# Kernel optimization log

Measured on AMD Instinct MI355X. Metric: run time of the kernel, lower is better.

The kernel has to match this reference:

```python
import jax, jax.numpy as jnp
import numpy as np

N, E = 100000, 600000
IN, H = 164, 128
NH = 4  # attention heads over embed_dim H//4 = 32


def layer_norm(x, g, b, eps=1e-5):
    m = x.mean(-1, keepdims=True)
    v = x.var(-1, keepdims=True)
    return (x - m) * jax.lax.rsqrt(v + eps) * g + b


def gcn_conv(x, W, b, src, dst, n):
    # PyG GCNConv: add self-loops, symmetric D^{-1/2}(A+I)D^{-1/2} normalization.
    deg = jnp.ones((n,), x.dtype).at[dst].add(1.0)  # degree of A+I on target nodes
    dinv = jax.lax.rsqrt(deg)
    xw = x @ W  # [n, out]
    msg = xw[src] * (dinv[src] * dinv[dst])[:, None]  # gather + edge-norm
    agg = jax.ops.segment_sum(msg, dst, num_segments=n)  # scatter-add
    agg = agg + xw * (dinv * dinv)[:, None]  # self-loop term
    return agg + b


def mha_seq1(x, Wq, bq, Wk, bk, Wv, bv, Wo, bo):
    # nn.MultiheadAttention with seq_len==1: softmax over a single key -> weights==1.
    dh = x.shape[-1] // NH
    q = (x @ Wq + bq).reshape(-1, NH, dh)
    k = (x @ Wk + bk).reshape(-1, NH, dh)
    v = (x @ Wv + bv).reshape(-1, NH, dh)
    scores = jnp.sum(q * k, -1, keepdims=True) / jnp.sqrt(jnp.float32(dh))  # [n,NH,1]
    attn = jax.nn.softmax(scores[..., None], axis=-1)[..., 0]  # all ones, kept for fidelity
    out = (attn * v).reshape(-1, NH * dh)
    return out @ Wo + bo


def setup_inputs() -> dict:
    key = jax.random.key(0)
    ks = jax.random.split(key, 16)

    def kaiming(k, i, o):
        return jax.random.normal(k, (i, o), jnp.float32) * (2.0 / i) ** 0.5

    Ha, Hb, Hc = H, H // 2, H // 4  # 128, 64, 32
    return {
        "x": jax.random.normal(ks[0], (N, IN), jnp.float32),
        "edge_index": jax.random.randint(ks[1], (2, E), 0, N),
        "Wi": kaiming(ks[2], IN, Ha), "bi": jnp.zeros((Ha,), jnp.float32),
        "g1": jnp.ones((Ha,), jnp.float32), "b1": jnp.zeros((Ha,), jnp.float32),
        "Wg1": kaiming(ks[3], Ha, Ha), "bg1": jnp.zeros((Ha,), jnp.float32),
        "Wg2": kaiming(ks[4], Ha, Hb), "bg2": jnp.zeros((Hb,), jnp.float32),
        "g2": jnp.ones((Hb,), jnp.float32), "b2": jnp.zeros((Hb,), jnp.float32),
        "Wg3": kaiming(ks[5], Hb, Hc), "bg3": jnp.zeros((Hc,), jnp.float32),
        "Wq": kaiming(ks[6], Hc, Hc), "bq": jnp.zeros((Hc,), jnp.float32),
        "Wk": kaiming(ks[7], Hc, Hc), "bk": jnp.zeros((Hc,), jnp.float32),
        "Wv": kaiming(ks[8], Hc, Hc), "bv": jnp.zeros((Hc,), jnp.float32),
        "Wo": kaiming(ks[9], Hc, Hc), "bo": jnp.zeros((Hc,), jnp.float32),
        "Wc1": kaiming(ks[10], Hc, H // 8), "bc1": jnp.zeros((H // 8,), jnp.float32),
        "Wc2": kaiming(ks[11], H // 8, 32), "bc2": jnp.zeros((32,), jnp.float32),
        "Wc3": kaiming(ks[12], 32, 1), "bc3": jnp.zeros((1,), jnp.float32),
    }


def reference(x, edge_index, Wi, bi, g1, b1, Wg1, bg1, Wg2, bg2, g2, b2,
              Wg3, bg3, Wq, bq, Wk, bk, Wv, bv, Wo, bo,
              Wc1, bc1, Wc2, bc2, Wc3, bc3):
    src, dst = edge_index[0], edge_index[1]
    n = x.shape[0]
    # dropout layers are identity in eval mode
    h = layer_norm(jax.nn.relu(x @ Wi + bi), g1, b1)
    h1 = jax.nn.relu(gcn_conv(h, Wg1, bg1, src, dst, n)) + h
    h2 = layer_norm(jax.nn.relu(gcn_conv(h1, Wg2, bg2, src, dst, n)), g2, b2)
    h3 = jax.nn.relu(gcn_conv(h2, Wg3, bg3, src, dst, n))
    h3 = mha_seq1(h3, Wq, bq, Wk, bk, Wv, bv, Wo, bo)
    h3 = jax.nn.relu(h3 @ Wc1 + bc1)
    h3 = jax.nn.relu(h3 @ Wc2 + bc2)
    return (h3 @ Wc3 + bc3)[:, 0]
```

## Files before the change

kernel.cpp:

```cpp
#include <hip/hip_runtime.h>


typedef __attribute__((ext_vector_type(8))) _Float16 f16x8;
typedef __attribute__((ext_vector_type(4))) _Float16 f16x4;
typedef __attribute__((ext_vector_type(4))) float f32x4;

#define GLOAD_LDS16(gp, lp)                                        \
  __builtin_amdgcn_global_load_lds(                                \
      (const __attribute__((address_space(1))) void*)(gp),         \
      (__attribute__((address_space(3))) void*)(lp), 16, 0, 0)

static __device__ __forceinline__ void wait_vm0() {
  asm volatile("s_waitcnt vmcnt(0)" ::: "memory");
}
static __device__ __forceinline__ void wait_vm1() {
  asm volatile("s_waitcnt vmcnt(1)" ::: "memory");
}
static __device__ __forceinline__ void wait_vm2() {
  asm volatile("s_waitcnt vmcnt(2)" ::: "memory");
}

__global__ void k_count(const int* __restrict__ dst, int* __restrict__ counts, int e) {
  int i = blockIdx.x * blockDim.x + threadIdx.x;
  if (i < e) atomicAdd(&counts[dst[i]], 1);
}

__global__ __launch_bounds__(256) void k_scan_part(
    const int* __restrict__ counts, int* __restrict__ bsums, int n) {
  int tid = threadIdx.x;
  int i0 = blockIdx.x * 1024 + tid * 4;
  int s = 0;
#pragma unroll
  for (int k = 0; k < 4; k++) { int i = i0 + k; if (i < n) s += counts[i]; }
#pragma unroll
  for (int d = 1; d < 64; d <<= 1) s += __shfl_xor(s, d);
  __shared__ int wsum[4];
  int lane = tid & 63, w = tid >> 6;
  if (lane == 0) wsum[w] = s;
  __syncthreads();
  if (tid == 0) bsums[blockIdx.x] = wsum[0] + wsum[1] + wsum[2] + wsum[3];
}

__global__ __launch_bounds__(128) void k_scan_top(int* __restrict__ bsums, int nb) {
  int tid = threadIdx.x;
  int orig = (tid < nb) ? bsums[tid] : 0;
  int v = orig;
  int lane = tid & 63, w = tid >> 6;
#pragma unroll
  for (int d = 1; d < 64; d <<= 1) { int t = __shfl_up(v, d); if (lane >= d) v += t; }
  __shared__ int ws[2];
  if (lane == 63) ws[w] = v;
  __syncthreads();
  if (w == 1) v += ws[0];
  if (tid < nb) bsums[tid] = v - orig;
}

__global__ __launch_bounds__(256) void k_scan_down(
    int* __restrict__ counts, const int* __restrict__ bsums,
    int* __restrict__ offsets, float* __restrict__ dinv, int n, int e) {
  int tid = threadIdx.x;
  int i0 = blockIdx.x * 1024 + tid * 4;
  int c[4]; int tsum = 0;
#pragma unroll
  for (int k = 0; k < 4; k++) { int i = i0 + k; c[k] = (i < n) ? counts[i] : 0; tsum += c[k]; }
  int v = tsum;
  int lane = tid & 63, w = tid >> 6;
#pragma unroll
  for (int d = 1; d < 64; d <<= 1) { int t = __shfl_up(v, d); if (lane >= d) v += t; }
  __shared__ int wsum[4];
  if (lane == 63) wsum[w] = v;
  __syncthreads();
  int wadd = 0;
#pragma unroll
  for (int q = 0; q < 4; q++) if (q < w) wadd += wsum[q];
  int run = (v - tsum) + wadd + bsums[blockIdx.x];
#pragma unroll
  for (int k = 0; k < 4; k++) {
    int i = i0 + k;
    if (i < n) {
      offsets[i] = run;
      dinv[i] = rsqrtf((float)(c[k] + 1));
      counts[i] = 0;
    }
    run += c[k];
  }
  if (blockIdx.x == 0 && tid == 0) offsets[n] = e;
}

__global__ void k_fill(const int* __restrict__ src, const int* __restrict__ dst,
                       const int* __restrict__ offsets, int* __restrict__ cursor,
                       const float* __restrict__ dinv, int2* __restrict__ csr, int e) {
  int i = blockIdx.x * blockDim.x + threadIdx.x;
  if (i >= e) return;
  int s = src[i], d = dst[i];
  int pos = atomicAdd(&cursor[d], 1);
  csr[offsets[d] + pos] = make_int2(s, __float_as_int(dinv[s] * dinv[d]));
}

__device__ __forceinline__ void pack_hi(const float* __restrict__ W,
                                        _Float16* __restrict__ dst,
                                        int K, int N, int u) {
  int lane = u & 63; int rest = u >> 6; int CT = N >> 4;
  int ct = rest % CT, ks = rest / CT;
  int gcol = ct * 16 + (lane & 15);
  int gk0 = ks * 32 + (lane >> 4) * 8;
  size_t o = (size_t)(ks * CT + ct) * 512 + lane * 8;
#pragma unroll
  for (int i = 0; i < 8; i++) {
    float v = (gk0 + i < K) ? W[(size_t)(gk0 + i) * N + gcol] : 0.0f;
    dst[o + i] = (_Float16)v;
  }
}

__global__ void k_setup(const float* __restrict__ Wi, const float* __restrict__ Wg1,
                        const float* __restrict__ Wg2, const float* __restrict__ Wg3,
                        _Float16* __restrict__ pWi, _Float16* __restrict__ pWg1,
                        _Float16* __restrict__ pWg2, _Float16* __restrict__ pWg3,
                        int* __restrict__ counts, float* __restrict__ zp, int n) {
  int b = blockIdx.x;
  if (b < 25) {
    int t = b * 256 + threadIdx.x;
    if (t < 3072) pack_hi(Wi, pWi, 164, 128, t);
    else if (t < 5120) pack_hi(Wg1, pWg1, 128, 128, t - 3072);
    else if (t < 6144) pack_hi(Wg2, pWg2, 128, 64, t - 5120);
    else if (t < 6400) pack_hi(Wg3, pWg3, 64, 32, t - 6144);
  } else {
    if (b == 25 && threadIdx.x < 64) zp[threadIdx.x] = 0.0f;
    int i = (b - 25) * 256 + threadIdx.x;
    if (i < n) counts[i] = 0;
  }
}

__global__ __launch_bounds__(512, 4) void k_gemm_in(
    const float* __restrict__ x, const _Float16* __restrict__ pB,
    const float* __restrict__ bias, const float* __restrict__ gamma,
    const float* __restrict__ beta, const float* __restrict__ zp,
    _Float16* __restrict__ out, int n) {
  constexpr int N = 128, CT = 8;
  __shared__ __align__(16) float sA[2][128 * 32];
  int tid = threadIdx.x;
  int lane = tid & 63, w = tid >> 6;
  int base = blockIdx.x * 128;
  const f16x8* Bf = (const f16x8*)pB;

  auto stage = [&](int ks, int buf) {
#pragma unroll
    for (int j = 0; j < 2; j++) {
      int q = (j * 8 + w) * 64 + lane;
      int row = q >> 3;
      int c = q & 7;
      int rg = base + row;
      const void* src = (rg < n && (ks < 5 || c == 0))
                            ? (const void*)(x + (size_t)rg * 164 + ks * 32 + c * 4)
                            : (const void*)zp;
      GLOAD_LDS16(src, &sA[buf][(size_t)(j * 8 + w) * 256]);
    }
  };

  f32x4 acc[CT];
#pragma unroll
  for (int c = 0; c < CT; c++) acc[c] = (f32x4)0.0f;

  stage(0, 0);
#pragma unroll
  for (int ks = 0; ks < 6; ks++) {
    if (ks + 1 < 6) { stage(ks + 1, (ks + 1) & 1); wait_vm2(); }
    else wait_vm0();
    __builtin_amdgcn_s_barrier();
    const float4* fr = (const float4*)&sA[ks & 1][((w * 16 + (lane & 15)) * 32) +
                                                 (lane >> 4) * 8];
    float4 u0 = fr[0], u1 = fr[1];
    float v[8] = {u0.x, u0.y, u0.z, u0.w, u1.x, u1.y, u1.z, u1.w};
    f16x8 ah, al;
#pragma unroll
    for (int i = 0; i < 8; i++) {
      ah[i] = (_Float16)v[i];
      al[i] = (_Float16)(v[i] - (float)ah[i]);
    }
#pragma unroll
    for (int c = 0; c < CT; c++) {
      f16x8 b = Bf[(ks * CT + c) * 64 + lane];
      acc[c] = __builtin_amdgcn_mfma_f32_16x16x32_f16(ah, b, acc[c], 0, 0, 0);
      acc[c] = __builtin_amdgcn_mfma_f32_16x16x32_f16(al, b, acc[c], 0, 0, 0);
    }
    __builtin_amdgcn_s_barrier();
  }

  int r0 = (lane >> 4) * 4;
  int li = lane & 15;
  float s1[4] = {0, 0, 0, 0}, s2[4] = {0, 0, 0, 0};
#pragma unroll
  for (int c = 0; c < CT; c++) {
    float bb = bias[c * 16 + li];
#pragma unroll
    for (int r = 0; r < 4; r++) {
      float t = acc[c][r] + bb;
      t = t > 0.0f ? t : 0.0f;
      acc[c][r] = t;
      s1[r] += t;
      s2[r] += t * t;
    }
  }
#pragma unroll
  for (int m = 1; m < 16; m <<= 1) {
#pragma unroll
    for (int r = 0; r < 4; r++) {
      s1[r] += __shfl_xor(s1[r], m);
      s2[r] += __shfl_xor(s2[r], m);
    }
  }
#pragma unroll
  for (int c = 0; c < CT; c++) {
    float gv = gamma[c * 16 + li], bv = beta[c * 16 + li];
#pragma unroll
    for (int r = 0; r < 4; r++) {
      int node = base + w * 16 + r0 + r;
      if (node < n) {
        float mean = s1[r] * (1.0f / N);
        float var = s2[r] * (1.0f / N) - mean * mean;
        float rs = rsqrtf(var + 1e-5f);
        out[(size_t)node * N + c * 16 + li] =
            (_Float16)((acc[c][r] - mean) * rs * gv + bv);
      }
    }
  }
}

template <int K, int N>
__global__ __launch_bounds__(512, 4) void k_gemm_f16(
    const _Float16* __restrict__ A, const _Float16* __restrict__ pB,
    const float* __restrict__ zp, _Float16* __restrict__ out, int n) {
  constexpr int KS = K / 32, CT = N / 16;
  __shared__ __align__(16) _Float16 sA[2][128 * 32];
  int tid = threadIdx.x;
  int lane = tid & 63, w = tid >> 6;
  int base = blockIdx.x * 128;
  const f16x8* Bf = (const f16x8*)pB;

  auto stage = [&](int ks, int buf) {
    int q = w * 64 + lane;
    int row = q >> 2;
    int c = q & 3;
    int rg = base + row;
    const void* src = (rg < n) ? (const void*)(A + (size_t)rg * K + ks * 32 + c * 8)
                               : (const void*)zp;
    GLOAD_LDS16(src, &sA[buf][(size_t)w * 512]);
  };

  f32x4 acc[CT];
#pragma unroll
  for (int c = 0; c < CT; c++) acc[c] = (f32x4)0.0f;

  stage(0, 0);
#pragma unroll
  for (int ks = 0; ks < KS; ks++) {
    if (ks + 1 < KS) { stage(ks + 1, (ks + 1) & 1); wait_vm1(); }
    else wait_vm0();
    __builtin_amdgcn_s_barrier();
    f16x8 av = *(const f16x8*)&sA[ks & 1][((w * 16 + (lane & 15)) * 32) +
                                          (lane >> 4) * 8];
#pragma unroll
    for (int c = 0; c < CT; c++) {
      f16x8 b = Bf[(ks * CT + c) * 64 + lane];
      acc[c] = __builtin_amdgcn_mfma_f32_16x16x32_f16(av, b, acc[c], 0, 0, 0);
    }
    __builtin_amdgcn_s_barrier();
  }

  int r0 = (lane >> 4) * 4;
  int li = lane & 15;
#pragma unroll
  for (int c = 0; c < CT; c++) {
#pragma unroll
    for (int r = 0; r < 4; r++) {
      int node = base + w * 16 + r0 + r;
      if (node < n) out[(size_t)node * N + c * 16 + li] = (_Float16)acc[c][r];
    }
  }
}

template <int OUT_D, int MODE>
__global__ __launch_bounds__(256, 2) void k_gather(
    const int* __restrict__ off, const int2* __restrict__ csr,
    const _Float16* __restrict__ xw, const float* __restrict__ dinv,
    const float* __restrict__ bias, const _Float16* __restrict__ auxh,
    const float* __restrict__ gamma, const float* __restrict__ beta,
    _Float16* __restrict__ out, int n) {
  constexpr int TPN = OUT_D / 4;
  constexpr int NPB = 256 / TPN;
  int tid = threadIdx.x;
  int node = blockIdx.x * NPB + tid / TPN;
  int li = tid % TPN;
  if (node >= n) return;
  int start = off[node], end = off[node + 1];
  float di = dinv[node];
  float d2 = di * di;
  const _Float16* xp = xw + 4 * li;
  f16x4 self = *(const f16x4*)(xp + (size_t)node * OUT_D);
  f16x4 hres;
  if constexpr (MODE == 0)
    hres = *(const f16x4*)(auxh + (size_t)node * OUT_D + 4 * li);
  float a0 = (float)self[0] * d2 + bias[4 * li + 0];
  float a1 = (float)self[1] * d2 + bias[4 * li + 1];
  float a2 = (float)self[2] * d2 + bias[4 * li + 2];
  float a3 = (float)self[3] * d2 + bias[4 * li + 3];
  for (int cb = start; cb < end; cb += TPN) {
    int m = end - cb; if (m > TPN) m = TPN;
    int sv = node; float nv = 0.0f;
    if (li < m) { int2 me = csr[cb + li]; sv = me.x; nv = __int_as_float(me.y); }
    for (int j0 = 0; j0 < m; j0 += 8) {
      int s0 = __shfl(sv, j0 + 0, TPN), s1 = __shfl(sv, j0 + 1, TPN);
      int s2 = __shfl(sv, j0 + 2, TPN), s3 = __shfl(sv, j0 + 3, TPN);
      int s4 = __shfl(sv, j0 + 4, TPN), s5 = __shfl(sv, j0 + 5, TPN);
      int s6 = __shfl(sv, j0 + 6, TPN), s7 = __shfl(sv, j0 + 7, TPN);
      float w0 = __shfl(nv, j0 + 0, TPN), w1 = __shfl(nv, j0 + 1, TPN);
      float w2 = __shfl(nv, j0 + 2, TPN), w3 = __shfl(nv, j0 + 3, TPN);
      float w4 = __shfl(nv, j0 + 4, TPN), w5 = __shfl(nv, j0 + 5, TPN);
      float w6 = __shfl(nv, j0 + 6, TPN), w7 = __shfl(nv, j0 + 7, TPN);
      f16x4 v0 = *(const f16x4*)(xp + (size_t)s0 * OUT_D);
      f16x4 v1 = *(const f16x4*)(xp + (size_t)s1 * OUT_D);
      f16x4 v2 = *(const f16x4*)(xp + (size_t)s2 * OUT_D);
      f16x4 v3 = *(const f16x4*)(xp + (size_t)s3 * OUT_D);
      f16x4 v4 = *(const f16x4*)(xp + (size_t)s4 * OUT_D);
      f16x4 v5 = *(const f16x4*)(xp + (size_t)s5 * OUT_D);
      f16x4 v6 = *(const f16x4*)(xp + (size_t)s6 * OUT_D);
      f16x4 v7 = *(const f16x4*)(xp + (size_t)s7 * OUT_D);
      a0 += (float)v0[0] * w0 + (float)v1[0] * w1 + (float)v2[0] * w2 + (float)v3[0] * w3
          + (float)v4[0] * w4 + (float)v5[0] * w5 + (float)v6[0] * w6 + (float)v7[0] * w7;
      a1 += (float)v0[1] * w0 + (float)v1[1] * w1 + (float)v2[1] * w2 + (float)v3[1] * w3
          + (float)v4[1] * w4 + (float)v5[1] * w5 + (float)v6[1] * w6 + (float)v7[1] * w7;
      a2 += (float)v0[2] * w0 + (float)v1[2] * w1 + (float)v2[2] * w2 + (float)v3[2] * w3
          + (float)v4[2] * w4 + (float)v5[2] * w5 + (float)v6[2] * w6 + (float)v7[2] * w7;
      a3 += (float)v0[3] * w0 + (float)v1[3] * w1 + (float)v2[3] * w2 + (float)v3[3] * w3
          + (float)v4[3] * w4 + (float)v5[3] * w5 + (float)v6[3] * w6 + (float)v7[3] * w7;
    }
  }
  _Float16* po = out + (size_t)node * OUT_D + 4 * li;
  if constexpr (MODE == 0) {
    f16x4 o;
    o[0] = (_Float16)((a0 > 0.0f ? a0 : 0.0f) + (float)hres[0]);
    o[1] = (_Float16)((a1 > 0.0f ? a1 : 0.0f) + (float)hres[1]);
    o[2] = (_Float16)((a2 > 0.0f ? a2 : 0.0f) + (float)hres[2]);
    o[3] = (_Float16)((a3 > 0.0f ? a3 : 0.0f) + (float)hres[3]);
    *(f16x4*)po = o;
  } else if constexpr (MODE == 1) {
    float v0 = a0 > 0.0f ? a0 : 0.0f, v1 = a1 > 0.0f ? a1 : 0.0f;
    float v2 = a2 > 0.0f ? a2 : 0.0f, v3 = a3 > 0.0f ? a3 : 0.0f;
    float s1 = v0 + v1 + v2 + v3;
    float s2 = v0 * v0 + v1 * v1 + v2 * v2 + v3 * v3;
#pragma unroll
    for (int d = 1; d < TPN; d <<= 1) {
      s1 += __shfl_xor(s1, d, TPN);
      s2 += __shfl_xor(s2, d, TPN);
    }
    float m_ = s1 * (1.0f / OUT_D);
    float var = s2 * (1.0f / OUT_D) - m_ * m_;
    float rs = rsqrtf(var + 1e-5f);
    f16x4 o;
    o[0] = (_Float16)((v0 - m_) * rs * gamma[4 * li + 0] + beta[4 * li + 0]);
    o[1] = (_Float16)((v1 - m_) * rs * gamma[4 * li + 1] + beta[4 * li + 1]);
    o[2] = (_Float16)((v2 - m_) * rs * gamma[4 * li + 2] + beta[4 * li + 2]);
    o[3] = (_Float16)((v3 - m_) * rs * gamma[4 * li + 3] + beta[4 * li + 3]);
    *(f16x4*)po = o;
  } else {
    f16x4 o;
    o[0] = (_Float16)a0; o[1] = (_Float16)a1;
    o[2] = (_Float16)a2; o[3] = (_Float16)a3;
    *(f16x4*)po = o;
  }
}

__global__ __launch_bounds__(256) void k_tail(
    const _Float16* __restrict__ agg3, const float* __restrict__ Wv,
    const float* __restrict__ bv, const float* __restrict__ Wo,
    const float* __restrict__ bo, const float* __restrict__ Wc1,
    const float* __restrict__ bc1, const float* __restrict__ Wc2,
    const float* __restrict__ bc2, const float* __restrict__ Wc3,
    const float* __restrict__ bc3, float* __restrict__ out, int n) {
  __shared__ float sWv[1024], sWo[1024], sWc1[512], sWc2[512];
  __shared__ float sbv[32], sbo[32], sbc2[32], sWc3[32], sbc1[16], sbc3[1];
  int tid = threadIdx.x;
  for (int i = tid; i < 1024; i += 256) { sWv[i] = Wv[i]; sWo[i] = Wo[i]; }
  for (int i = tid; i < 512; i += 256) { sWc1[i] = Wc1[i]; sWc2[i] = Wc2[i]; }
  if (tid < 32) { sbv[tid] = bv[tid]; sbo[tid] = bo[tid];
                  sbc2[tid] = bc2[tid]; sWc3[tid] = Wc3[tid]; }
  if (tid < 16) sbc1[tid] = bc1[tid];
  if (tid == 0) sbc3[0] = bc3[0];
  __syncthreads();
  int node = blockIdx.x * blockDim.x + tid;
  if (node >= n) return;
  float a[32];
  const f16x8* row8 = (const f16x8*)(agg3 + (size_t)node * 32);
#pragma unroll
  for (int q = 0; q < 4; q++) {
    f16x8 t = row8[q];
#pragma unroll
    for (int i = 0; i < 8; i++) {
      float f = (float)t[i];
      a[8 * q + i] = f > 0.0f ? f : 0.0f;
    }
  }
  float v[32];
#pragma unroll
  for (int j = 0; j < 32; j++) v[j] = sbv[j];
  for (int k = 0; k < 32; k++) {
#pragma unroll
    for (int j = 0; j < 32; j++) v[j] += a[k] * sWv[k * 32 + j];
  }
  float o[32];
#pragma unroll
  for (int j = 0; j < 32; j++) o[j] = sbo[j];
  for (int k = 0; k < 32; k++) {
#pragma unroll
    for (int j = 0; j < 32; j++) o[j] += v[k] * sWo[k * 32 + j];
  }
  float c1[16];
#pragma unroll
  for (int j = 0; j < 16; j++) c1[j] = sbc1[j];
  for (int k = 0; k < 32; k++) {
#pragma unroll
    for (int j = 0; j < 16; j++) c1[j] += o[k] * sWc1[k * 16 + j];
  }
#pragma unroll
  for (int j = 0; j < 16; j++) c1[j] = c1[j] > 0.0f ? c1[j] : 0.0f;
  float c2[32];
#pragma unroll
  for (int j = 0; j < 32; j++) c2[j] = sbc2[j];
  for (int k = 0; k < 16; k++) {
#pragma unroll
    for (int j = 0; j < 32; j++) c2[j] += c1[k] * sWc2[k * 32 + j];
  }
  float r = sbc3[0];
#pragma unroll
  for (int k = 0; k < 32; k++) {
    float c = c2[k] > 0.0f ? c2[k] : 0.0f;
    r += c * sWc3[k];
  }
  out[node] = r;
}

extern "C" void kernel_launch(void* const* d_in, const int* in_sizes, int n_in,
                              void* d_out, int out_size, void* d_ws, size_t ws_size,
                              hipStream_t stream) {
  const float* x   = (const float*)d_in[0];
  const int* ei    = (const int*)d_in[1];
  const float* Wi  = (const float*)d_in[2];
  const float* bi  = (const float*)d_in[3];
  const float* g1  = (const float*)d_in[4];
  const float* b1  = (const float*)d_in[5];
  const float* Wg1 = (const float*)d_in[6];
  const float* bg1 = (const float*)d_in[7];
  const float* Wg2 = (const float*)d_in[8];
  const float* bg2 = (const float*)d_in[9];
  const float* g2  = (const float*)d_in[10];
  const float* b2  = (const float*)d_in[11];
  const float* Wg3 = (const float*)d_in[12];
  const float* bg3 = (const float*)d_in[13];
  const float* Wv  = (const float*)d_in[18];
  const float* bv  = (const float*)d_in[19];
  const float* Wo  = (const float*)d_in[20];
  const float* bo  = (const float*)d_in[21];
  const float* Wc1 = (const float*)d_in[22];
  const float* bc1 = (const float*)d_in[23];
  const float* Wc2 = (const float*)d_in[24];
  const float* bc2 = (const float*)d_in[25];
  const float* Wc3 = (const float*)d_in[26];
  const float* bc3 = (const float*)d_in[27];

  const int n = in_sizes[0] / 164;
  const int e = in_sizes[1] / 2;
  const int* src = ei;
  const int* dst = ei + e;

  char* ws = (char*)d_ws;
  size_t off = 0;
  auto alloc = [&](size_t bytes) {
    char* p = ws + off;
    off += (bytes + 255) & ~(size_t)255;
    return p;
  };
  _Float16* A     = (_Float16*)alloc((size_t)n * 128 * 2);
  _Float16* B     = (_Float16*)alloc((size_t)n * 128 * 2);
  _Float16* C     = (_Float16*)alloc((size_t)n * 128 * 2);
  float* dinv     = (float*)alloc((size_t)n * 4);
  int*   counts   = (int*)alloc((size_t)n * 4);
  int*   offsets  = (int*)alloc((size_t)(n + 1) * 4);
  int*   bsums    = (int*)alloc(128 * 4);
  int2*  csr      = (int2*)alloc((size_t)e * 8);
  _Float16* pWi   = (_Float16*)alloc(3072 * 16);
  _Float16* pWg1  = (_Float16*)alloc(2048 * 16);
  _Float16* pWg2  = (_Float16*)alloc(1024 * 16);
  _Float16* pWg3  = (_Float16*)alloc(256 * 16);
  float* zp       = (float*)alloc(64 * 4);
  (void)ws_size;

  const int BS = 256;
  const int SB = (n + 1023) / 1024;
  const int GB = (n + 127) / 128;

  k_setup<<<25 + (n + 255) / 256, 256, 0, stream>>>(
      Wi, Wg1, Wg2, Wg3, pWi, pWg1, pWg2, pWg3, counts, zp, n);

  k_count<<<(e + BS - 1) / BS, BS, 0, stream>>>(dst, counts, e);
  k_scan_part<<<SB, 256, 0, stream>>>(counts, bsums, n);
  k_scan_top<<<1, 128, 0, stream>>>(bsums, SB);
  k_scan_down<<<SB, 256, 0, stream>>>(counts, bsums, offsets, dinv, n, e);
  k_fill<<<(e + BS - 1) / BS, BS, 0, stream>>>(src, dst, offsets, counts, dinv,
                                               csr, e);

  k_gemm_in<<<GB, 512, 0, stream>>>(x, pWi, bi, g1, b1, zp, A, n);

  k_gemm_f16<128, 128><<<GB, 512, 0, stream>>>(A, pWg1, zp, B, n);
  k_gather<128, 0><<<(n + 7) / 8, 256, 0, stream>>>(
      offsets, csr, B, dinv, bg1, A, nullptr, nullptr, C, n);

  k_gemm_f16<128, 64><<<GB, 512, 0, stream>>>(C, pWg2, zp, A, n);
  k_gather<64, 1><<<(n + 15) / 16, 256, 0, stream>>>(
      offsets, csr, A, dinv, bg2, nullptr, g2, b2, B, n);

  k_gemm_f16<64, 32><<<GB, 512, 0, stream>>>(B, pWg3, zp, A, n);
  k_gather<32, 2><<<(n + 31) / 32, 256, 0, stream>>>(
      offsets, csr, A, dinv, bg3, nullptr, nullptr, nullptr, C, n);

  k_tail<<<(n + BS - 1) / BS, BS, 0, stream>>>(
      C, Wv, bv, Wo, bo, Wc1, bc1, Wc2, bc2, Wc3, bc3, (float*)d_out, n);
}
```

Before: 237.0 us.

## Use per-wave LDS tiles with XOR swizzle and drop block barriers in GEMMs

Each wave now stages only its own 16 rows into a private LDS slice. This removes the two block-wide s_barrier calls per K-step in both the input GEMM and the f16 GEMM. The LDS column chunks are XOR-swizzled by row to avoid bank conflicts on fragment reads, and the B fragments for each K-step are loaded into registers before the async A stage is issued. In exchange, register pressure rises from holding eight B fragments, and correctness depends on each wave's own vmcnt waits covering the LDS writes.

```diff
diff --git a/kernel.cpp b/kernel.cpp
--- a/kernel.cpp
+++ b/kernel.cpp
@@ -137,23 +137,22 @@
     const float* __restrict__ beta, const float* __restrict__ zp,
     _Float16* __restrict__ out, int n) {
   constexpr int N = 128, CT = 8;
-  __shared__ __align__(16) float sA[2][128 * 32];
+  __shared__ __align__(16) float sAi[8][2][512];
   int tid = threadIdx.x;
   int lane = tid & 63, w = tid >> 6;
-  int base = blockIdx.x * 128;
+  int rowbase = blockIdx.x * 128 + w * 16;
   const f16x8* Bf = (const f16x8*)pB;
 
   auto stage = [&](int ks, int buf) {
 #pragma unroll
     for (int j = 0; j < 2; j++) {
-      int q = (j * 8 + w) * 64 + lane;
-      int row = q >> 3;
-      int c = q & 7;
-      int rg = base + row;
-      const void* src = (rg < n && (ks < 5 || c == 0))
-                            ? (const void*)(x + (size_t)rg * 164 + ks * 32 + c * 4)
-                            : (const void*)zp;
-      GLOAD_LDS16(src, &sA[buf][(size_t)(j * 8 + w) * 256]);
+      int r_ = j * 8 + (lane >> 3);
+      int c_ = (lane & 7) ^ (lane >> 3);
+      int rg = rowbase + r_;
+      bool ok = (rg < n) && (ks < 5 || c_ == 0);
+      const void* s = ok ? (const void*)(x + (size_t)rg * 164 + ks * 32 + c_ * 4)
+                         : (const void*)zp;
+      GLOAD_LDS16(s, &sAi[w][buf][j * 256]);
     }
   };
 
@@ -161,15 +160,22 @@
 #pragma unroll
   for (int c = 0; c < CT; c++) acc[c] = (f32x4)0.0f;
 
+  int rr = lane & 15;
+  int c0 = (lane >> 4) * 2;
+  int s0 = c0 ^ (rr & 7);
+  int s1 = (c0 + 1) ^ (rr & 7);
+
   stage(0, 0);
 #pragma unroll
   for (int ks = 0; ks < 6; ks++) {
+    f16x8 bfr[CT];
+#pragma unroll
+    for (int c = 0; c < CT; c++) bfr[c] = Bf[(ks * CT + c) * 64 + lane];
     if (ks + 1 < 6) { stage(ks + 1, (ks + 1) & 1); wait_vm2(); }
     else wait_vm0();
-    __builtin_amdgcn_s_barrier();
-    const float4* fr = (const float4*)&sA[ks & 1][((w * 16 + (lane & 15)) * 32) +
-                                                 (lane >> 4) * 8];
-    float4 u0 = fr[0], u1 = fr[1];
+    const float* bp = &sAi[w][ks & 1][0];
+    float4 u0 = *(const float4*)&bp[rr * 32 + s0 * 4];
+    float4 u1 = *(const float4*)&bp[rr * 32 + s1 * 4];
     float v[8] = {u0.x, u0.y, u0.z, u0.w, u1.x, u1.y, u1.z, u1.w};
     f16x8 ah, al;
 #pragma unroll
@@ -179,16 +185,14 @@
     }
 #pragma unroll
     for (int c = 0; c < CT; c++) {
-      f16x8 b = Bf[(ks * CT + c) * 64 + lane];
-      acc[c] = __builtin_amdgcn_mfma_f32_16x16x32_f16(ah, b, acc[c], 0, 0, 0);
-      acc[c] = __builtin_amdgcn_mfma_f32_16x16x32_f16(al, b, acc[c], 0, 0, 0);
-    }
-    __builtin_amdgcn_s_barrier();
+      acc[c] = __builtin_amdgcn_mfma_f32_16x16x32_f16(ah, bfr[c], acc[c], 0, 0, 0);
+      acc[c] = __builtin_amdgcn_mfma_f32_16x16x32_f16(al, bfr[c], acc[c], 0, 0, 0);
+    }
   }
 
   int r0 = (lane >> 4) * 4;
   int li = lane & 15;
-  float s1[4] = {0, 0, 0, 0}, s2[4] = {0, 0, 0, 0};
+  float s1v[4] = {0, 0, 0, 0}, s2v[4] = {0, 0, 0, 0};
 #pragma unroll
   for (int c = 0; c < CT; c++) {
     float bb = bias[c * 16 + li];
@@ -197,16 +201,16 @@
       float t = acc[c][r] + bb;
       t = t > 0.0f ? t : 0.0f;
       acc[c][r] = t;
-      s1[r] += t;
-      s2[r] += t * t;
+      s1v[r] += t;
+      s2v[r] += t * t;
     }
   }
 #pragma unroll
   for (int m = 1; m < 16; m <<= 1) {
 #pragma unroll
     for (int r = 0; r < 4; r++) {
-      s1[r] += __shfl_xor(s1[r], m);
-      s2[r] += __shfl_xor(s2[r], m);
+      s1v[r] += __shfl_xor(s1v[r], m);
+      s2v[r] += __shfl_xor(s2v[r], m);
     }
   }
 #pragma unroll
@@ -214,10 +218,10 @@
     float gv = gamma[c * 16 + li], bv = beta[c * 16 + li];
 #pragma unroll
     for (int r = 0; r < 4; r++) {
-      int node = base + w * 16 + r0 + r;
+      int node = rowbase + r0 + r;
       if (node < n) {
-        float mean = s1[r] * (1.0f / N);
-        float var = s2[r] * (1.0f / N) - mean * mean;
+        float mean = s1v[r] * (1.0f / N);
+        float var = s2v[r] * (1.0f / N) - mean * mean;
         float rs = rsqrtf(var + 1e-5f);
         out[(size_t)node * N + c * 16 + li] =
             (_Float16)((acc[c][r] - mean) * rs * gv + bv);
@@ -231,40 +235,43 @@
     const _Float16* __restrict__ A, const _Float16* __restrict__ pB,
     const float* __restrict__ zp, _Float16* __restrict__ out, int n) {
   constexpr int KS = K / 32, CT = N / 16;
-  __shared__ __align__(16) _Float16 sA[2][128 * 32];
+  __shared__ __align__(16) _Float16 sA[8][2][512];
   int tid = threadIdx.x;
   int lane = tid & 63, w = tid >> 6;
-  int base = blockIdx.x * 128;
+  int rowbase = blockIdx.x * 128 + w * 16;
   const f16x8* Bf = (const f16x8*)pB;
 
+  int r_ = lane >> 2;
+  int c_ = (lane & 3) ^ (r_ & 3);
+  int rg = rowbase + r_;
+  const _Float16* asrc = A + (size_t)rg * K + c_ * 8;
+  bool rok = rg < n;
+
   auto stage = [&](int ks, int buf) {
-    int q = w * 64 + lane;
-    int row = q >> 2;
-    int c = q & 3;
-    int rg = base + row;
-    const void* src = (rg < n) ? (const void*)(A + (size_t)rg * K + ks * 32 + c * 8)
-                               : (const void*)zp;
-    GLOAD_LDS16(src, &sA[buf][(size_t)w * 512]);
+    const void* s = rok ? (const void*)(asrc + ks * 32) : (const void*)zp;
+    GLOAD_LDS16(s, &sA[w][buf][0]);
   };
 
   f32x4 acc[CT];
 #pragma unroll
   for (int c = 0; c < CT; c++) acc[c] = (f32x4)0.0f;
 
+  int rr = lane & 15;
+  int slot = (lane >> 4) ^ (rr & 3);
+
   stage(0, 0);
 #pragma unroll
   for (int ks = 0; ks < KS; ks++) {
+    f16x8 bfr[CT];
+#pragma unroll
+    for (int c = 0; c < CT; c++) bfr[c] = Bf[(ks * CT + c) * 64 + lane];
     if (ks + 1 < KS) { stage(ks + 1, (ks + 1) & 1); wait_vm1(); }
     else wait_vm0();
-    __builtin_amdgcn_s_barrier();
-    f16x8 av = *(const f16x8*)&sA[ks & 1][((w * 16 + (lane & 15)) * 32) +
-                                          (lane >> 4) * 8];
+    f16x8 av = *(const f16x8*)&sA[w][ks & 1][rr * 32 + slot * 8];
 #pragma unroll
     for (int c = 0; c < CT; c++) {
-      f16x8 b = Bf[(ks * CT + c) * 64 + lane];
-      acc[c] = __builtin_amdgcn_mfma_f32_16x16x32_f16(av, b, acc[c], 0, 0, 0);
-    }
-    __builtin_amdgcn_s_barrier();
+      acc[c] = __builtin_amdgcn_mfma_f32_16x16x32_f16(av, bfr[c], acc[c], 0, 0, 0);
+    }
   }
 
   int r0 = (lane >> 4) * 4;
@@ -273,7 +280,7 @@
   for (int c = 0; c < CT; c++) {
 #pragma unroll
     for (int r = 0; r < 4; r++) {
-      int node = base + w * 16 + r0 + r;
+      int node = rowbase + r0 + r;
       if (node < n) out[(size_t)node * N + c * 16 + li] = (_Float16)acc[c][r];
     }
   }
```

Result: faster. 227.4 us (-4.0%).
